# Kernel optimization log

Measured on AMD Instinct MI355X. Metric: run time of the kernel, lower is better.

## Reference

```python
import jax, jax.numpy as jnp
import numpy as np

B, H, W = 16, 540, 960


def setup_inputs() -> dict:
    key = jax.random.key(0)
    k1, k2, k3, k4 = jax.random.split(key, 4)
    return {
        "flowAB": jax.random.normal(k1, (B, 2, H, W), dtype=jnp.float32),
        "back_flowAB": jax.random.normal(k2, (B, 2, H, W), dtype=jnp.float32),
        "flowBC": jax.random.normal(k3, (B, 2, H, W), dtype=jnp.float32),
        "imgB_depth": jax.random.uniform(k4, (B, 1, H, W), dtype=jnp.float32),
    }


def _depth_aware_forward_warp(flowBC, back_flowAB, imgB_depth):
    # Forward-warp (splat) flowBC to frame A using back_flowAB as the
    # displacement, weighting contributions by exp(-depth) so nearer
    # surfaces dominate (depth-aware occlusion handling), then normalize.
    b, _, h, w = flowBC.shape
    dt = flowBC.dtype
    xx = jnp.arange(w, dtype=dt)[None, None, :]   # [1,1,W]
    yy = jnp.arange(h, dtype=dt)[None, :, None]   # [1,H,1]
    tx = xx + back_flowAB[:, 0]                   # [B,H,W] target x
    ty = yy + back_flowAB[:, 1]                   # [B,H,W] target y
    x0 = jnp.floor(tx)
    y0 = jnp.floor(ty)

    dw = jnp.exp(-imgB_depth[:, 0])               # [B,H,W] occlusion weight
    ones = jnp.ones((b, 1, h, w), dt)
    vals = jnp.concatenate([flowBC, ones], axis=1) * dw[:, None]  # [B,3,H,W]

    acc = jnp.zeros((b * h * w, 3), dt)
    boff = (jnp.arange(b) * h * w)[:, None, None]  # batch offset into flat grid
    for ox, oy in ((0, 0), (1, 0), (0, 1), (1, 1)):  # 4 bilinear corners
        xi = x0 + ox
        yi = y0 + oy
        wgt = (1.0 - jnp.abs(tx - xi)) * (1.0 - jnp.abs(ty - yi))
        valid = (xi >= 0) & (xi < w) & (yi >= 0) & (yi < h)
        wgt = jnp.where(valid, wgt, 0.0)
        idx = (boff
               + jnp.clip(yi, 0, h - 1).astype(jnp.int32) * w
               + jnp.clip(xi, 0, w - 1).astype(jnp.int32)).reshape(-1)
        contrib = (vals * wgt[:, None]).transpose(0, 2, 3, 1).reshape(-1, 3)
        acc = acc.at[idx].add(contrib)

    acc = acc.reshape(b, h, w, 3)
    den = acc[..., 2:3]
    eps = jnp.asarray(1e-6, dt)
    warped = jnp.where(den > eps, acc[..., :2] / jnp.maximum(den, eps), 0.0)
    return warped.transpose(0, 3, 1, 2)  # [B,2,H,W]


def reference(flowAB, back_flowAB, flowBC, imgB_depth):
    concat_flow = _depth_aware_forward_warp(flowBC, back_flowAB, imgB_depth)
    return concat_flow + flowAB
```

## Files before the change

kernel.cpp:

```cpp
#include <hip/hip_runtime.h>
#include <hip/hip_fp16.h>

#define BB 16
#define HH 540
#define WW 960
static constexpr int HW = HH * WW;

#define TW 64
#define TH 64
#define HALO 7
#define RW (TW + 2 * HALO)
#define RH (TH + 2 * HALO)
#define RCELLS (RW * RH)
#define TCX 15
#define TCY 9

#define FP_SCALE 67108864.0f
#define FP_INV   (1.0f / 67108864.0f)

#define SPLAT_THREADS 1024


__global__ __launch_bounds__(SPLAT_THREADS) void splat_tile_kernel(
    const float* __restrict__ back_flow,
    const float* __restrict__ flowBC,
    const float* __restrict__ depth,
    uint2* __restrict__ regions)
{
    __shared__ unsigned long long accA[RCELLS];
    __shared__ int                accB[RCELLS];

    const int tcx = blockIdx.x;
    const int tcy = blockIdx.y;
    const int b   = blockIdx.z;
    const int tx0 = tcx * TW;
    const int ty0 = tcy * TH;

    for (int i = threadIdx.x; i < RCELLS; i += SPLAT_THREADS) {
        accA[i] = 0ull;
        accB[i] = 0;
    }
    __syncthreads();

    const float* bfp = back_flow + (size_t)b * 2 * HW;
    const float* fcp = flowBC    + (size_t)b * 2 * HW;
    const float* dp  = depth     + (size_t)b * HW;

    const int row  = threadIdx.x >> 4;
    const int colb = (threadIdx.x & 15) << 2;
    const int y    = ty0 + row;

    if (y < HH) {
        const int t0 = y * WW + tx0 + colb;

        float bx[4], by[4], f0[4], f1[4], dz[4];
        *(float4*)bx = *(const float4*)(bfp + t0);
        *(float4*)by = *(const float4*)(bfp + HW + t0);
        *(float4*)f0 = *(const float4*)(fcp + t0);
        *(float4*)f1 = *(const float4*)(fcp + HW + t0);
        *(float4*)dz = *(const float4*)(dp + t0);

#pragma unroll
        for (int k = 0; k < 4; ++k) {
            const int x = tx0 + colb + k;

            const float txf = (float)x + bx[k];
            const float tyf = (float)y + by[k];
            const float dw  = __expf(-dz[k]);
            const float v0s = f0[k] * dw * FP_SCALE;
            const float v1s = f1[k] * dw * FP_SCALE;
            const float dws = dw * FP_SCALE;

            const float x0f = floorf(txf);
            const float y0f = floorf(tyf);
            const float fx  = txf - x0f;
            const float fy  = tyf - y0f;

            int rx = (int)x0f - tx0 + HALO;
            int ry = (int)y0f - ty0 + HALO;
            rx = min(max(rx, 0), RW - 2);
            ry = min(max(ry, 0), RH - 2);

            const float gx0 = 1.0f - fx, gy0 = 1.0f - fy;
            const float w00 = gx0 * gy0, w10 = fx * gy0;
            const float w01 = gx0 * fy,  w11 = fx * fy;

            const int c00 = ry * RW + rx;
            const int c01 = c00 + RW;

#define SPLAT_CORNER(ci, w)                                                  \
            {                                                                \
                const long long pk =                                         \
                    ((long long)(int)(v0s * (w)) << 32) |                    \
                    (unsigned int)__float2uint_rn(dws * (w));                \
                atomicAdd(&accA[ci], (unsigned long long)pk);                \
                atomicAdd(&accB[ci], (int)(v1s * (w)));                      \
            }

            SPLAT_CORNER(c00,     w00)
            SPLAT_CORNER(c00 + 1, w10)
            SPLAT_CORNER(c01,     w01)
            SPLAT_CORNER(c01 + 1, w11)
#undef SPLAT_CORNER
        }
    }

    __syncthreads();
    const size_t base = (((size_t)b * TCY + tcy) * TCX + tcx) * (size_t)RCELLS;
    for (int i = threadIdx.x; i < RCELLS; i += SPLAT_THREADS) {
        const unsigned long long a = accA[i];
        const float v0  = (float)(int)(a >> 32)  * FP_INV;
        const float den = (float)(unsigned int)a * FP_INV;
        const float v1  = (float)accB[i]         * FP_INV;
        const __half2 h = __floats2half2_rn(v0, v1);
        uint2 cell;
        cell.x = *(const unsigned int*)&h;
        cell.y = __float_as_uint(den);
        regions[base + i] = cell;
    }
}

__global__ __launch_bounds__(256) void finalize_tiles_kernel(
    const uint2* __restrict__ regions,
    const float* __restrict__ flowAB,
    float* __restrict__ out)
{
    const int t0 = (blockIdx.x * 256 + threadIdx.x) * 4;
    const int b  = blockIdx.y;
    if (t0 >= HW) return;

    const int y   = t0 / WW;
    const int x0  = t0 - y * WW;
    const int cty = y >> 6;
    const int ly  = y - cty * TH;

    int ty2 = -1;
    if (ly < HALO)            ty2 = cty - 1;
    else if (ly >= TH - HALO) ty2 = cty + 1;
    if (ty2 < 0 || ty2 >= TCY) ty2 = -1;

    const size_t brow  = (size_t)b * TCY;
    const int    ryA   = ly + HALO;
    const int    ryB   = (ty2 >= 0) ? (y - ty2 * TH + HALO) : 0;

    float a0[4], a1[4], a2[4];

#pragma unroll
    for (int k = 0; k < 4; ++k) {
        const int x   = x0 + k;
        const int ctx = x >> 6;
        const int lx  = x - ctx * TW;

        int tx2 = -1;
        if (lx < HALO)            tx2 = ctx - 1;
        else if (lx >= TW - HALO) tx2 = ctx + 1;
        if (tx2 < 0 || tx2 >= TCX) tx2 = -1;

        float s0 = 0.0f, s1 = 0.0f, s2 = 0.0f;

#define GATHER(tcy_, ry_, tcx_)                                              \
        {                                                                    \
            const int rx_ = x - (tcx_) * TW + HALO;                          \
            const uint2 c = regions[((brow + (tcy_)) * TCX + (tcx_)) *       \
                                    (size_t)RCELLS + (ry_) * RW + rx_];      \
            const __half2 h = *(const __half2*)&c.x;                         \
            const float2 f = __half22float2(h);                              \
            s0 += f.x;                                                       \
            s1 += f.y;                                                       \
            s2 += __uint_as_float(c.y);                                      \
        }

        GATHER(cty, ryA, ctx)
        if (tx2 >= 0)              GATHER(cty, ryA, tx2)
        if (ty2 >= 0)              GATHER(ty2, ryB, ctx)
        if (ty2 >= 0 && tx2 >= 0)  GATHER(ty2, ryB, tx2)
#undef GATHER

        a0[k] = s0; a1[k] = s1; a2[k] = s2;
    }

    float4 r0, r1;
    const float4 fA = *(const float4*)(flowAB + (size_t)b * 2 * HW + t0);
    const float4 fB = *(const float4*)(flowAB + (size_t)b * 2 * HW + HW + t0);
#pragma unroll
    for (int k = 0; k < 4; ++k) {
        const float inv = (a2[k] > 1e-6f) ? (1.0f / a2[k]) : 0.0f;
        (&r0.x)[k] = a0[k] * inv + (&fA.x)[k];
        (&r1.x)[k] = a1[k] * inv + (&fB.x)[k];
    }
    *(float4*)(out + (size_t)b * 2 * HW + t0)      = r0;
    *(float4*)(out + (size_t)b * 2 * HW + HW + t0) = r1;
}

__global__ __launch_bounds__(256) void splat_kernel(
    const float* __restrict__ back_flow,
    const float* __restrict__ flowBC,
    const float* __restrict__ depth,
    float* __restrict__ acc)
{
    int t = blockIdx.x * blockDim.x + threadIdx.x;
    int b = blockIdx.y;
    if (t >= HW) return;
    int y = t / WW;
    int x = t - y * WW;
    const float* bfp = back_flow + (size_t)b * 2 * HW;
    const float* fcp = flowBC    + (size_t)b * 2 * HW;
    float tx = (float)x + bfp[t];
    float ty = (float)y + bfp[t + HW];
    float dw = expf(-depth[(size_t)b * HW + t]);
    float v0 = fcp[t] * dw;
    float v1 = fcp[t + HW] * dw;
    float x0f = floorf(tx), y0f = floorf(ty);
    int x0 = (int)x0f, y0 = (int)y0f;
    float fx = tx - x0f, fy = ty - y0f;
    float wx[2] = {1.0f - fx, fx};
    float wy[2] = {1.0f - fy, fy};
    float* accb = acc + (size_t)b * HW * 3;
#pragma unroll
    for (int oy = 0; oy < 2; ++oy) {
        int yi = y0 + oy;
        if (yi < 0 || yi >= HH) continue;
#pragma unroll
        for (int ox = 0; ox < 2; ++ox) {
            int xi = x0 + ox;
            if (xi < 0 || xi >= WW) continue;
            float wgt = wx[ox] * wy[oy];
            if (wgt == 0.0f) continue;
            float* p = accb + ((size_t)yi * WW + xi) * 3;
            atomicAdd(p + 0, v0 * wgt);
            atomicAdd(p + 1, v1 * wgt);
            atomicAdd(p + 2, dw * wgt);
        }
    }
}

__global__ __launch_bounds__(256) void finalize_kernel(
    const float* __restrict__ acc,
    const float* __restrict__ flowAB,
    float* __restrict__ out)
{
    int t = blockIdx.x * blockDim.x + threadIdx.x;
    int b = blockIdx.y;
    if (t >= HW) return;
    const float* p = acc + ((size_t)b * HW + t) * 3;
    float a0 = p[0], a1 = p[1], den = p[2];
    float inv = (den > 1e-6f) ? (1.0f / den) : 0.0f;
    size_t o = (size_t)b * 2 * HW + t;
    out[o]      = a0 * inv + flowAB[o];
    out[o + HW] = a1 * inv + flowAB[o + HW];
}

extern "C" void kernel_launch(void* const* d_in, const int* in_sizes, int n_in,
                              void* d_out, int out_size, void* d_ws, size_t ws_size,
                              hipStream_t stream) {
    const float* flowAB    = (const float*)d_in[0];
    const float* back_flow = (const float*)d_in[1];
    const float* flowBC    = (const float*)d_in[2];
    const float* depth     = (const float*)d_in[3];
    float* out = (float*)d_out;

    const size_t regions_bytes =
        (size_t)BB * TCY * TCX * (size_t)RCELLS * sizeof(uint2);

    if (ws_size >= regions_bytes) {
        uint2* regions = (uint2*)d_ws;
        dim3 sgrid(TCX, TCY, BB);
        splat_tile_kernel<<<sgrid, SPLAT_THREADS, 0, stream>>>(back_flow, flowBC, depth, regions);
        dim3 fgrid((HW / 4 + 255) / 256, BB);
        finalize_tiles_kernel<<<fgrid, 256, 0, stream>>>(regions, flowAB, out);
    } else {
        float* acc = (float*)d_ws;
        size_t acc_bytes = (size_t)BB * HW * 3 * sizeof(float);
        hipMemsetAsync(acc, 0, acc_bytes, stream);
        dim3 grid((HW + 255) / 256, BB);
        splat_kernel<<<grid, 256, 0, stream>>>(back_flow, flowBC, depth, acc);
        finalize_kernel<<<grid, 256, 0, stream>>>(acc, flowAB, out);
    }
}
```

Before: 110.4 us.

## Finalize tile interiors in splat kernel, gather only boundary pixels separately

The splat kernel now writes only the halo-affected ring of each region buffer to global memory and finalizes interior pixels (which no neighbor tile can touch) directly from shared memory, adding flowAB and writing the output. A new boundary finalize kernel handles only the 7-pixel border strips of each tile, gathering from up to four neighboring regions. This removes most of the region-buffer round trip and the full-image gather pass. The cost is more complex index mapping, uncoalesced scalar stores in the boundary kernel, and extra work in the splat kernel's tail.

```diff
diff --git a/kernel.cpp b/kernel.cpp
--- a/kernel.cpp
+++ b/kernel.cpp
@@ -12,6 +12,7 @@
 #define RW (TW + 2 * HALO)
 #define RH (TH + 2 * HALO)
 #define RCELLS (RW * RH)
+#define SCELLS 3584
 #define TCX 15
 #define TCY 9
 
@@ -25,7 +26,9 @@
     const float* __restrict__ back_flow,
     const float* __restrict__ flowBC,
     const float* __restrict__ depth,
-    uint2* __restrict__ regions)
+    const float* __restrict__ flowAB,
+    uint2* __restrict__ regions,
+    float* __restrict__ out)
 {
     __shared__ unsigned long long accA[RCELLS];
     __shared__ int                accB[RCELLS];
@@ -106,90 +109,117 @@
     }
 
     __syncthreads();
+
     const size_t base = (((size_t)b * TCY + tcy) * TCX + tcx) * (size_t)RCELLS;
-    for (int i = threadIdx.x; i < RCELLS; i += SPLAT_THREADS) {
-        const unsigned long long a = accA[i];
+    for (int i = threadIdx.x; i < SCELLS; i += SPLAT_THREADS) {
+        int ry, rx;
+        if (i < 2184) {
+            ry = i / 78;  rx = i - ry * 78;
+            if (ry >= 14) ry += 50;
+        } else {
+            const int j = i - 2184;
+            const int r = j / 28;
+            const int c = j - r * 28;
+            ry = 14 + r;
+            rx = (c < 14) ? c : c + 50;
+        }
+        const int cell = ry * RW + rx;
+        const unsigned long long a = accA[cell];
         const float v0  = (float)(int)(a >> 32)  * FP_INV;
         const float den = (float)(unsigned int)a * FP_INV;
-        const float v1  = (float)accB[i]         * FP_INV;
+        const float v1  = (float)accB[cell]      * FP_INV;
         const __half2 h = __floats2half2_rn(v0, v1);
-        uint2 cell;
-        cell.x = *(const unsigned int*)&h;
-        cell.y = __float_as_uint(den);
-        regions[base + i] = cell;
-    }
-}
-
-__global__ __launch_bounds__(256) void finalize_tiles_kernel(
+        uint2 cellv;
+        cellv.x = *(const unsigned int*)&h;
+        cellv.y = __float_as_uint(den);
+        regions[base + cell] = cellv;
+    }
+
+    for (int i = threadIdx.x; i < 2500; i += SPLAT_THREADS) {
+        const int r  = i / 50;
+        const int c  = i - r * 50;
+        const int ly = 7 + r;
+        const int lx = 7 + c;
+        const int yy = ty0 + ly;
+        if (yy >= HH) continue;
+        const int cell = (ly + HALO) * RW + (lx + HALO);
+        const unsigned long long a = accA[cell];
+        const float v0  = (float)(int)(a >> 32)  * FP_INV;
+        const float den = (float)(unsigned int)a * FP_INV;
+        const float v1  = (float)accB[cell]      * FP_INV;
+        const float inv = (den > 1e-6f) ? (1.0f / den) : 0.0f;
+        const size_t o  = (size_t)b * 2 * HW + (size_t)yy * WW + (tx0 + lx);
+        out[o]      = v0 * inv + flowAB[o];
+        out[o + HW] = v1 * inv + flowAB[o + HW];
+    }
+}
+
+__global__ __launch_bounds__(256) void finalize_boundary_kernel(
     const uint2* __restrict__ regions,
     const float* __restrict__ flowAB,
     float* __restrict__ out)
 {
-    const int t0 = (blockIdx.x * 256 + threadIdx.x) * 4;
-    const int b  = blockIdx.y;
-    if (t0 >= HW) return;
-
-    const int y   = t0 / WW;
-    const int x0  = t0 - y * WW;
-    const int cty = y >> 6;
-    const int ly  = y - cty * TH;
-
+    const int tid = blockIdx.x * 256 + threadIdx.x;
+    if (tid >= 1596) return;
+    const int tile = blockIdx.y;
+    const int b    = blockIdx.z;
+    const int tcy  = tile / TCX;
+    const int tcx  = tile - tcy * TCX;
+
+    int lx, ly;
+    if (tid < 896) {
+        const int r = tid >> 6;
+        lx = tid & 63;
+        ly = (r < 7) ? r : r + 50;
+    } else {
+        const int j = tid - 896;
+        const int r = j / 14;
+        const int c = j - r * 14;
+        ly = 7 + r;
+        lx = (c < 7) ? c : c + 50;
+    }
+
+    const int x = tcx * TW + lx;
+    const int y = tcy * TH + ly;
+    if (y >= HH) return;
+
+    int tx2 = -1;
+    if (lx < HALO)            tx2 = tcx - 1;
+    else if (lx >= TW - HALO) tx2 = tcx + 1;
+    if (tx2 < 0 || tx2 >= TCX) tx2 = -1;
     int ty2 = -1;
-    if (ly < HALO)            ty2 = cty - 1;
-    else if (ly >= TH - HALO) ty2 = cty + 1;
+    if (ly < HALO)            ty2 = tcy - 1;
+    else if (ly >= TH - HALO) ty2 = tcy + 1;
     if (ty2 < 0 || ty2 >= TCY) ty2 = -1;
 
-    const size_t brow  = (size_t)b * TCY;
-    const int    ryA   = ly + HALO;
-    const int    ryB   = (ty2 >= 0) ? (y - ty2 * TH + HALO) : 0;
-
-    float a0[4], a1[4], a2[4];
-
-#pragma unroll
-    for (int k = 0; k < 4; ++k) {
-        const int x   = x0 + k;
-        const int ctx = x >> 6;
-        const int lx  = x - ctx * TW;
-
-        int tx2 = -1;
-        if (lx < HALO)            tx2 = ctx - 1;
-        else if (lx >= TW - HALO) tx2 = ctx + 1;
-        if (tx2 < 0 || tx2 >= TCX) tx2 = -1;
-
-        float s0 = 0.0f, s1 = 0.0f, s2 = 0.0f;
+    const size_t brow = (size_t)b * TCY;
+    const int ryA = ly + HALO;
+    const int ryB = (ty2 >= 0) ? (y - ty2 * TH + HALO) : 0;
+
+    float s0 = 0.0f, s1 = 0.0f, s2 = 0.0f;
 
 #define GATHER(tcy_, ry_, tcx_)                                              \
-        {                                                                    \
-            const int rx_ = x - (tcx_) * TW + HALO;                          \
-            const uint2 c = regions[((brow + (tcy_)) * TCX + (tcx_)) *       \
-                                    (size_t)RCELLS + (ry_) * RW + rx_];      \
-            const __half2 h = *(const __half2*)&c.x;                         \
-            const float2 f = __half22float2(h);                              \
-            s0 += f.x;                                                       \
-            s1 += f.y;                                                       \
-            s2 += __uint_as_float(c.y);                                      \
-        }
-
-        GATHER(cty, ryA, ctx)
-        if (tx2 >= 0)              GATHER(cty, ryA, tx2)
-        if (ty2 >= 0)              GATHER(ty2, ryB, ctx)
-        if (ty2 >= 0 && tx2 >= 0)  GATHER(ty2, ryB, tx2)
+    {                                                                        \
+        const int rx_ = x - (tcx_) * TW + HALO;                              \
+        const uint2 cv = regions[((brow + (tcy_)) * TCX + (tcx_)) *          \
+                                 (size_t)RCELLS + (ry_) * RW + rx_];         \
+        const __half2 h = *(const __half2*)&cv.x;                            \
+        const float2 f = __half22float2(h);                                  \
+        s0 += f.x;                                                           \
+        s1 += f.y;                                                           \
+        s2 += __uint_as_float(cv.y);                                         \
+    }
+
+    GATHER(tcy, ryA, tcx)
+    if (tx2 >= 0)              GATHER(tcy, ryA, tx2)
+    if (ty2 >= 0)              GATHER(ty2, ryB, tcx)
+    if (ty2 >= 0 && tx2 >= 0)  GATHER(ty2, ryB, tx2)
 #undef GATHER
 
-        a0[k] = s0; a1[k] = s1; a2[k] = s2;
-    }
-
-    float4 r0, r1;
-    const float4 fA = *(const float4*)(flowAB + (size_t)b * 2 * HW + t0);
-    const float4 fB = *(const float4*)(flowAB + (size_t)b * 2 * HW + HW + t0);
-#pragma unroll
-    for (int k = 0; k < 4; ++k) {
-        const float inv = (a2[k] > 1e-6f) ? (1.0f / a2[k]) : 0.0f;
-        (&r0.x)[k] = a0[k] * inv + (&fA.x)[k];
-        (&r1.x)[k] = a1[k] * inv + (&fB.x)[k];
-    }
-    *(float4*)(out + (size_t)b * 2 * HW + t0)      = r0;
-    *(float4*)(out + (size_t)b * 2 * HW + HW + t0) = r1;
+    const float inv = (s2 > 1e-6f) ? (1.0f / s2) : 0.0f;
+    const size_t o = (size_t)b * 2 * HW + (size_t)y * WW + x;
+    out[o]      = s0 * inv + flowAB[o];
+    out[o + HW] = s1 * inv + flowAB[o + HW];
 }
 
 __global__ __launch_bounds__(256) void splat_kernel(
@@ -265,9 +295,10 @@
     if (ws_size >= regions_bytes) {
         uint2* regions = (uint2*)d_ws;
         dim3 sgrid(TCX, TCY, BB);
-        splat_tile_kernel<<<sgrid, SPLAT_THREADS, 0, stream>>>(back_flow, flowBC, depth, regions);
-        dim3 fgrid((HW / 4 + 255) / 256, BB);
-        finalize_tiles_kernel<<<fgrid, 256, 0, stream>>>(regions, flowAB, out);
+        splat_tile_kernel<<<sgrid, SPLAT_THREADS, 0, stream>>>(
+            back_flow, flowBC, depth, flowAB, regions, out);
+        dim3 fgrid(7, TCX * TCY, BB);
+        finalize_boundary_kernel<<<fgrid, 256, 0, stream>>>(regions, flowAB, out);
     } else {
         float* acc = (float*)d_ws;
         size_t acc_bytes = (size_t)BB * HW * 3 * sizeof(float);
```

After: 99.25 us. 10.1% less time.
